# Optimization experiments

Hardware: AMD Instinct MI355X
Metric: run time of the kernel (lower is better)

## Reference

```python
import jax, jax.numpy as jnp
import numpy as np

HIDDEN = 4096
NUM_HEADS = 32
NUM_KV_HEADS = 8
HEAD_DIM = HIDDEN // NUM_HEADS  # 128
Q_SIZE = NUM_HEADS * HEAD_DIM    # 4096
KV_SIZE = NUM_KV_HEADS * HEAD_DIM  # 1024
SCALE = 1.0 / HEAD_DIM  # attention_multiplier=None -> head_dim ** (-1)
ROPE_BASE = 10000.0


def _rope_neox(x, positions):
    # x: [B, S, H, D], positions: [B, S] int
    half = HEAD_DIM // 2
    inv_freq = 1.0 / (ROPE_BASE ** (jnp.arange(0, half, dtype=jnp.float32) / half))
    freqs = positions.astype(jnp.float32)[..., None] * inv_freq  # [B, S, half]
    cos = jnp.cos(freqs)[:, :, None, :]  # [B, S, 1, half]
    sin = jnp.sin(freqs)[:, :, None, :]
    x1, x2 = x[..., :half], x[..., half:]
    return jnp.concatenate([x1 * cos - x2 * sin, x2 * cos + x1 * sin], axis=-1)


def setup_inputs() -> dict:
    key = jax.random.key(0)
    k1, k2, k3 = jax.random.split(key, 3)
    B, S = 2, 2048
    positions = jnp.broadcast_to(jnp.arange(S, dtype=jnp.int32), (B, S))
    hidden_states = jax.random.normal(k1, (B, S, HIDDEN), dtype=jnp.float32) * 0.02
    w_qkv = jax.random.normal(k2, (Q_SIZE + 2 * KV_SIZE, HIDDEN), dtype=jnp.float32) * 0.02
    w_o = jax.random.normal(k3, (HIDDEN, Q_SIZE), dtype=jnp.float32) * 0.02
    return {"positions": positions, "hidden_states": hidden_states, "w_qkv": w_qkv, "w_o": w_o}


def reference(positions, hidden_states, w_qkv, w_o):
    B, S, _ = hidden_states.shape
    # fused QKV projection
    qkv = jnp.einsum('bsh,oh->bso', hidden_states, w_qkv)
    q = qkv[..., :Q_SIZE].reshape(B, S, NUM_HEADS, HEAD_DIM)
    k = qkv[..., Q_SIZE:Q_SIZE + KV_SIZE].reshape(B, S, NUM_KV_HEADS, HEAD_DIM)
    v = qkv[..., Q_SIZE + KV_SIZE:].reshape(B, S, NUM_KV_HEADS, HEAD_DIM)
    # neox-style RoPE on q and k
    q = _rope_neox(q, positions)
    k = _rope_neox(k, positions)
    # GQA: repeat kv heads
    rep = NUM_HEADS // NUM_KV_HEADS
    k = jnp.repeat(k, rep, axis=2)  # [B, S, NUM_HEADS, D]
    v = jnp.repeat(v, rep, axis=2)
    # causal attention
    scores = jnp.einsum('bqhd,bkhd->bhqk', q, k) * SCALE
    causal = jnp.tril(jnp.ones((S, S), dtype=bool))
    scores = jnp.where(causal, scores, jnp.finfo(scores.dtype).min)
    probs = jax.nn.softmax(scores, axis=-1)
    attn = jnp.einsum('bhqk,bkhd->bqhd', probs, v).reshape(B, S, Q_SIZE)
    # output projection
    return jnp.einsum('bsq,hq->bsh', attn, w_o)
```

## Files before the change

### kernel.cpp

```cpp
#include <hip/hip_runtime.h>
#include <hip/hip_bf16.h>
#include <cmath>

typedef __bf16 bf16x8 __attribute__((ext_vector_type(8)));
typedef __bf16 bf16x4 __attribute__((ext_vector_type(4)));
typedef float  f32x4  __attribute__((ext_vector_type(4)));
typedef unsigned int u32;
typedef u32 u32x4 __attribute__((ext_vector_type(4)));

#define AS1 __attribute__((address_space(1)))
#define AS3 __attribute__((address_space(3)))
#define GLDS16(gp, lp) __builtin_amdgcn_global_load_lds((AS1 void*)(gp), (AS3 void*)(lp), 16, 0, 0)

#define B_DIM 2
#define S_LEN 2048
#define HIDDEN 4096
#define NHEADS 32
#define NKV 8
#define HDIM 128
#define QSZ 4096
#define KVSZ 1024
#define QKVSZ 6144
#define GK 4096
#define ATT_SCALE 0.0078125f
#define L2E 1.4426950408889634f

__global__ __launch_bounds__(256) void conv_f32_bf16(const float* __restrict__ in,
                                                     __bf16* __restrict__ out, int n4) {
    int idx = blockIdx.x * 256 + threadIdx.x;
    if (idx < n4) {
        float4 v = ((const float4*)in)[idx];
        bf16x4 o;
        o[0] = (__bf16)v.x; o[1] = (__bf16)v.y; o[2] = (__bf16)v.z; o[3] = (__bf16)v.w;
        ((bf16x4*)out)[idx] = o;
    }
}

__global__ __launch_bounds__(256) void rope_table_kernel(float* __restrict__ ct,
                                                         float* __restrict__ st) {
    int idx = blockIdx.x * 256 + threadIdx.x;
    int p = idx >> 6, i = idx & 63;
    float inv = expf(-(float)i * (9.210340371976184f / 64.0f));
    float freq = (float)p * inv;
    float s, c;
    sincosf(freq, &s, &c);
    ct[idx] = c; st[idx] = s;
}

template<typename OUT>
__global__ __launch_bounds__(512, 2) void gemm256(const __bf16* __restrict__ A,
                                                  const __bf16* __restrict__ B,
                                                  OUT* __restrict__ C,
                                                  int N) {
    __shared__ __bf16 Asm[2 * 16384 + 2 * 16384];
    char* Bbase = (char*)Asm + 65536;

    const int tid = threadIdx.x;
    const int w = tid >> 6, l = tid & 63;
    const int l15 = l & 15, l4 = l >> 4;
    const int wr = w >> 2, wc = w & 3;

    const int nwg = gridDim.x * gridDim.y;
    const int orig = blockIdx.y * gridDim.x + blockIdx.x;
    const int swz = (orig & 7) * (nwg >> 3) + (orig >> 3);
    const int bx = swz % gridDim.x, by = swz / gridDim.x;
    const int m0 = by * 256, n0 = bx * 256;

    const __bf16* Ag = A + (size_t)m0 * GK;
    const __bf16* Bg = B + (size_t)n0 * GK;

#define STAGE_AQ(q, tile) do {                                                  \
        int c_ = (q) * 512 + tid;                                               \
        int r_ = c_ >> 3;                                                       \
        int jg_ = (tid & 7) ^ (r_ & 7);                                         \
        GLDS16(Ag + (size_t)r_ * GK + (tile) * 64 + jg_ * 8,                    \
               (char*)Asm + ((tile) & 1) * 32768 + c_ * 16);                    \
    } while (0)
#define STAGE_BS(s, tile) do {                                                  \
        _Pragma("unroll")                                                       \
        for (int i_ = 0; i_ < 2; ++i_) {                                        \
            int v_ = i_ * 512 + tid;                                            \
            int r_ = (v_ >> 8) * 64 + (s) * 32 + ((v_ >> 3) & 31);              \
            int jg_ = (v_ & 7) ^ (r_ & 7);                                      \
            int c_ = r_ * 8 + (v_ & 7);                                         \
            GLDS16(Bg + (size_t)r_ * GK + (tile) * 64 + jg_ * 8,                \
                   Bbase + ((tile) & 1) * 32768 + c_ * 16);                     \
        }                                                                       \
    } while (0)

#define LOAD_A(DST, MH) do {                                                    \
        _Pragma("unroll")                                                       \
        for (int m2 = 0; m2 < 4; ++m2) {                                        \
            int row = wr * 128 + ((MH) * 4 + m2) * 16 + l15;                    \
            _Pragma("unroll")                                                   \
            for (int kk = 0; kk < 2; ++kk) {                                    \
                int j = (kk * 4 + l4) ^ (row & 7);                              \
                DST[m2][kk] = *(const bf16x8*)(Als + row * 64 + j * 8);         \
            }                                                                   \
        }                                                                       \
    } while (0)
#define LOAD_B(DST, NH) do {                                                    \
        _Pragma("unroll")                                                       \
        for (int n2 = 0; n2 < 2; ++n2) {                                        \
            int row = wc * 64 + ((NH) * 2 + n2) * 16 + l15;                     \
            _Pragma("unroll")                                                   \
            for (int kk = 0; kk < 2; ++kk) {                                    \
                int j = (kk * 4 + l4) ^ (row & 7);                              \
                DST[n2][kk] = *(const bf16x8*)(Bls + row * 64 + j * 8);         \
            }                                                                   \
        }                                                                       \
    } while (0)
#define MFMA_QUAD(AF, BF, MI0, NI0)                                             \
    _Pragma("unroll")                                                           \
    for (int m2 = 0; m2 < 4; ++m2)                                              \
        _Pragma("unroll")                                                       \
        for (int n2 = 0; n2 < 2; ++n2)                                          \
            _Pragma("unroll")                                                   \
            for (int kk = 0; kk < 2; ++kk)                                      \
                acc[(MI0) + m2][(NI0) + n2] =                                   \
                    __builtin_amdgcn_mfma_f32_16x16x32_bf16(                    \
                        AF[m2][kk], BF[n2][kk], acc[(MI0) + m2][(NI0) + n2], 0, 0, 0);
#define PH_SYNC_PRE  do { __builtin_amdgcn_sched_barrier(0);                    \
        __builtin_amdgcn_s_barrier();                                           \
        asm volatile("s_waitcnt lgkmcnt(0)" ::: "memory");                      \
        __builtin_amdgcn_sched_barrier(0); } while (0)
#define PH_SYNC_POST do { __builtin_amdgcn_sched_barrier(0);                    \
        __builtin_amdgcn_s_barrier(); } while (0)

    f32x4 acc[8][4] = {};

    const int T = GK / 64;
    STAGE_AQ(0, 0); STAGE_AQ(1, 0); STAGE_AQ(2, 0); STAGE_AQ(3, 0);
    STAGE_BS(0, 0); STAGE_BS(1, 0);
    STAGE_AQ(0, 1); STAGE_AQ(2, 1); STAGE_BS(0, 1);
    asm volatile("s_waitcnt vmcnt(4)" ::: "memory");
    __builtin_amdgcn_s_barrier();

    for (int t = 0; t < T; ++t) {
        const __bf16* Als = Asm + (t & 1) * 16384;
        const __bf16* Bls = (__bf16*)Bbase + (t & 1) * 16384;
        bf16x8 af0[4][2], af1[4][2], bfr[2][2];
        LOAD_A(af0, 0);
        LOAD_B(bfr, 0);
        if (t + 1 < T) { STAGE_AQ(1, t + 1); STAGE_AQ(3, t + 1); }
        PH_SYNC_PRE;
        __builtin_amdgcn_s_setprio(1);
        MFMA_QUAD(af0, bfr, 0, 0);
        __builtin_amdgcn_s_setprio(0);
        PH_SYNC_POST;
        LOAD_B(bfr, 1);
        if (t + 1 < T) STAGE_BS(1, t + 1);
        PH_SYNC_PRE;
        __builtin_amdgcn_s_setprio(1);
        MFMA_QUAD(af0, bfr, 0, 2);
        __builtin_amdgcn_s_setprio(0);
        PH_SYNC_POST;
        LOAD_A(af1, 1);
        LOAD_B(bfr, 0);
        if (t + 2 < T) { STAGE_AQ(0, t + 2); STAGE_AQ(2, t + 2); }
        PH_SYNC_PRE;
        __builtin_amdgcn_s_setprio(1);
        MFMA_QUAD(af1, bfr, 4, 0);
        __builtin_amdgcn_s_setprio(0);
        PH_SYNC_POST;
        LOAD_B(bfr, 1);
        if (t + 2 < T) STAGE_BS(0, t + 2);
        PH_SYNC_PRE;
        __builtin_amdgcn_s_setprio(1);
        MFMA_QUAD(af1, bfr, 4, 2);
        __builtin_amdgcn_s_setprio(0);
        if (t + 2 < T)      { asm volatile("s_waitcnt vmcnt(4)" ::: "memory"); }
        else if (t + 1 < T) { asm volatile("s_waitcnt vmcnt(0)" ::: "memory"); }
        PH_SYNC_POST;
    }
#undef PH_SYNC_PRE
#undef PH_SYNC_POST
#undef MFMA_QUAD
#undef LOAD_A
#undef LOAD_B
#undef STAGE_AQ
#undef STAGE_BS

#pragma unroll
    for (int mi = 0; mi < 8; ++mi)
#pragma unroll
        for (int ni = 0; ni < 4; ++ni)
#pragma unroll
            for (int r = 0; r < 4; ++r)
                C[(size_t)(m0 + wr * 128 + mi * 16 + l4 * 4 + r) * N
                  + n0 + wc * 64 + ni * 16 + l15] = (OUT)acc[mi][ni][r];
}

__global__ __launch_bounds__(256) void rope_kernel(const __bf16* __restrict__ qkv,
                                                   const int* __restrict__ pos,
                                                   const float* __restrict__ ct,
                                                   const float* __restrict__ st,
                                                   __bf16* __restrict__ Qb,
                                                   __bf16* __restrict__ Kb) {
    const int tid = threadIdx.x;
    const int tok = blockIdx.x;
    const int b = tok >> 11, s = tok & 2047;
    const int p = pos[tok];
    const __bf16* base = qkv + (size_t)tok * QKVSZ;
    const float* cb = ct + (size_t)p * 64;
    const float* sb = st + (size_t)p * 64;
    for (int idx = tid; idx < 2560; idx += 256) {
        int head = idx >> 6, i = idx & 63;
        float c = cb[i], sn = sb[i];
        if (head < 32) {
            float x1 = (float)base[head * HDIM + i];
            float x2 = (float)base[head * HDIM + 64 + i];
            size_t o = ((size_t)(b * 32 + head) * S_LEN + s) * HDIM + i;
            Qb[o]      = (__bf16)((x1 * c - x2 * sn) * ATT_SCALE);
            Qb[o + 64] = (__bf16)((x2 * c + x1 * sn) * ATT_SCALE);
        } else {
            int g = head - 32;
            float x1 = (float)base[QSZ + g * HDIM + i];
            float x2 = (float)base[QSZ + g * HDIM + 64 + i];
            size_t o = ((size_t)(b * 8 + g) * S_LEN + s) * HDIM + i;
            Kb[o]      = (__bf16)(x1 * c - x2 * sn);
            Kb[o + 64] = (__bf16)(x2 * c + x1 * sn);
        }
    }
}

__global__ __launch_bounds__(256) void vtrans_kernel(const __bf16* __restrict__ qkv,
                                                     __bf16* __restrict__ Vt) {
    __shared__ __bf16 T[64][132];
    const int tid = threadIdx.x;
    const int st = blockIdx.x, g = blockIdx.y, b = blockIdx.z;
    const __bf16* src = qkv + ((size_t)(b * S_LEN + st * 64)) * QKVSZ + (QSZ + KVSZ) + g * HDIM;
#pragma unroll
    for (int it = 0; it < 8; ++it) {
        int c = it * 256 + tid;
        int row = c >> 5;
        int c4 = c & 31;
        bf16x4 v = *(const bf16x4*)(src + (size_t)row * QKVSZ + c4 * 4);
        *(bf16x4*)(&T[row][c4 * 4]) = v;
    }
    __syncthreads();
#pragma unroll
    for (int it = 0; it < 8; ++it) {
        int c = it * 256 + tid;
        int d = c >> 4;
        int s4 = (c & 15) * 4;
        bf16x4 o;
        o[0] = T[s4 + 0][d]; o[1] = T[s4 + 1][d]; o[2] = T[s4 + 2][d]; o[3] = T[s4 + 3][d];
        *(bf16x4*)(Vt + ((size_t)(b * 8 + g) * HDIM + d) * S_LEN + st * 64 + s4) = o;
    }
}

__global__ __launch_bounds__(256, 2) void attn_kernel(const __bf16* __restrict__ Q,
                                                      const __bf16* __restrict__ K,
                                                      const __bf16* __restrict__ Vt,
                                                      __bf16* __restrict__ O) {
    const int tid = threadIdx.x;
    const int w = tid >> 6, l = tid & 63;
    const int l15 = l & 15, l4 = l >> 4;
    const int qt = gridDim.x - 1 - blockIdx.x;
    const int h = blockIdx.y, b = blockIdx.z;
    const int g = h >> 2;
    const int qw0 = qt * 128 + w * 32;

    __shared__ __bf16 Ks[2][64 * 128];
    __shared__ __bf16 Vs[2][128 * 64];

    const __bf16* Qp = Q + ((size_t)((b * 32 + h) * S_LEN + qw0)) * HDIM;
    const __bf16* Kp = K + (size_t)(b * 8 + g) * S_LEN * HDIM;
    const __bf16* Vp = Vt + (size_t)(b * 8 + g) * HDIM * S_LEN;

    bf16x8 qf[2][4];
#pragma unroll
    for (int qh = 0; qh < 2; ++qh)
#pragma unroll
        for (int kk = 0; kk < 4; ++kk)
            qf[qh][kk] = *(const bf16x8*)(Qp + (size_t)(qh * 16 + l15) * HDIM + kk * 32 + l4 * 8);

    f32x4 acc[2][8] = {};
    float m[2]    = {-1e30f, -1e30f};
    float lsum[2] = {0.f, 0.f};
    const bool oddl4 = (l4 & 1);

#define STAGE(buf, ktile) do {                                                     \
        const __bf16* kbase = Kp + (size_t)(ktile) * 64 * HDIM;                    \
        _Pragma("unroll")                                                          \
        for (int i_ = 0; i_ < 4; ++i_) {                                           \
            int c_ = i_ * 256 + tid;                \
            int row_ = c_ >> 4, cc_ = (c_ & 15) ^ (row_ & 7);                      \
            GLDS16(kbase + (size_t)row_ * HDIM + cc_ * 8,                          \
                   (char*)Ks[buf] + c_ * 16);                                      \
        }                                                                          \
        const __bf16* vbase = Vp + (size_t)(ktile) * 64;                           \
        _Pragma("unroll")                                                          \
        for (int i_ = 0; i_ < 4; ++i_) {                                           \
            int c_ = i_ * 256 + tid;                \
            int row_ = c_ >> 3, cc_ = (c_ & 7) ^ (row_ & 7);                       \
            GLDS16(vbase + (size_t)row_ * S_LEN + cc_ * 8,                         \
                   (char*)Vs[buf] + c_ * 16);                                      \
        }                                                                          \
    } while (0)

    const int nkt = 2 * qt + 2;
    int cur = 0;
    STAGE(0, 0);
    __syncthreads();

    for (int kt = 0; kt < nkt; ++kt) {
        if (kt + 1 < nkt) STAGE(cur ^ 1, kt + 1);
        if (kt * 64 <= qw0 + 31) {
            f32x4 sfr[2][4];
            __builtin_amdgcn_s_setprio(1);
#pragma unroll
            for (int fn = 0; fn < 4; ++fn) {
                f32x4 sa0 = {}, sa1 = {};
#pragma unroll
                for (int kk = 0; kk < 4; ++kk) {
                    int row = fn * 16 + l15;
                    int cc = (kk * 4 + l4) ^ (l15 & 7);
                    bf16x8 kb = *(const bf16x8*)(Ks[cur] + row * HDIM + cc * 8);
                    sa0 = __builtin_amdgcn_mfma_f32_16x16x32_bf16(kb, qf[0][kk], sa0, 0, 0, 0);
                    sa1 = __builtin_amdgcn_mfma_f32_16x16x32_bf16(kb, qf[1][kk], sa1, 0, 0, 0);
                }
                sfr[0][fn] = sa0; sfr[1][fn] = sa1;
            }
            __builtin_amdgcn_s_setprio(0);
            const bool needmask = (kt * 64 + 63 > qw0);
            bf16x8 pb[2][2];
#pragma unroll
            for (int qh = 0; qh < 2; ++qh) {
                const int qrow = qw0 + qh * 16 + l15;
                float pmax = -1e30f;
#pragma unroll
                for (int fn = 0; fn < 4; ++fn)
#pragma unroll
                    for (int r = 0; r < 4; ++r) {
                        float v = sfr[qh][fn][r];
                        if (needmask) {
                            int kcol = kt * 64 + fn * 16 + l4 * 4 + r;
                            if (kcol > qrow) v = -1e30f;
                        }
                        sfr[qh][fn][r] = v;
                        pmax = fmaxf(pmax, v);
                    }
                pmax = fmaxf(pmax, __shfl_xor(pmax, 16));
                pmax = fmaxf(pmax, __shfl_xor(pmax, 32));
                if (!__all(pmax - m[qh] <= 8.0f)) {
                    float mn = fmaxf(m[qh], pmax);
                    float alpha = exp2f((m[qh] - mn) * L2E);
                    m[qh] = mn;
                    lsum[qh] *= alpha;
#pragma unroll
                    for (int n = 0; n < 8; ++n)
#pragma unroll
                        for (int r = 0; r < 4; ++r) acc[qh][n][r] *= alpha;
                }
                float rs = 0.f;
                u32 pk01[4], pk23[4];
#pragma unroll
                for (int fn = 0; fn < 4; ++fn) {
                    float p0 = exp2f((sfr[qh][fn][0] - m[qh]) * L2E);
                    float p1 = exp2f((sfr[qh][fn][1] - m[qh]) * L2E);
                    float p2 = exp2f((sfr[qh][fn][2] - m[qh]) * L2E);
                    float p3 = exp2f((sfr[qh][fn][3] - m[qh]) * L2E);
                    rs += (p0 + p1) + (p2 + p3);
                    asm("v_cvt_pk_bf16_f32 %0, %1, %2" : "=v"(pk01[fn]) : "v"(p0), "v"(p1));
                    asm("v_cvt_pk_bf16_f32 %0, %1, %2" : "=v"(pk23[fn]) : "v"(p2), "v"(p3));
                }
                rs += __shfl_xor(rs, 16);
                rs += __shfl_xor(rs, 32);
                lsum[qh] += rs;
#pragma unroll
                for (int kk = 0; kk < 2; ++kk) {
                    u32 a01 = pk01[2 * kk],     a23 = pk23[2 * kk];
                    u32 b01 = pk01[2 * kk + 1], b23 = pk23[2 * kk + 1];
                    asm("v_permlane32_swap_b32 %0, %1" : "+v"(a01), "+v"(b01));
                    asm("v_permlane32_swap_b32 %0, %1" : "+v"(a23), "+v"(b23));
                    u32 oa01 = __shfl_xor(a01, 16);
                    u32 oa23 = __shfl_xor(a23, 16);
                    u32 ob01 = __shfl_xor(b01, 16);
                    u32 ob23 = __shfl_xor(b23, 16);
                    u32x4 wv;
                    wv[0] = oddl4 ? ob01 : a01;
                    wv[1] = oddl4 ? ob23 : a23;
                    wv[2] = oddl4 ? b01 : oa01;
                    wv[3] = oddl4 ? b23 : oa23;
                    pb[qh][kk] = __builtin_bit_cast(bf16x8, wv);
                }
            }
            __builtin_amdgcn_s_setprio(1);
#pragma unroll
            for (int kk = 0; kk < 2; ++kk) {
#pragma unroll
                for (int n = 0; n < 8; ++n) {
                    int row = n * 16 + l15;
                    int cc = (kk * 4 + l4) ^ (l15 & 7);
                    bf16x8 vb = *(const bf16x8*)(Vs[cur] + row * 64 + cc * 8);
                    acc[0][n] = __builtin_amdgcn_mfma_f32_16x16x32_bf16(vb, pb[0][kk], acc[0][n], 0, 0, 0);
                    acc[1][n] = __builtin_amdgcn_mfma_f32_16x16x32_bf16(vb, pb[1][kk], acc[1][n], 0, 0, 0);
                }
            }
            __builtin_amdgcn_s_setprio(0);
        }
        __syncthreads();
        cur ^= 1;
    }
#undef STAGE
#pragma unroll
    for (int qh = 0; qh < 2; ++qh) {
        float inv = 1.0f / lsum[qh];
        int qrow = qw0 + qh * 16 + l15;
        __bf16* obase = O + ((size_t)(b * S_LEN) + qrow) * QSZ + h * HDIM + l4 * 4;
#pragma unroll
        for (int n = 0; n < 8; ++n) {
            bf16x4 o4;
#pragma unroll
            for (int r = 0; r < 4; ++r) o4[r] = (__bf16)(acc[qh][n][r] * inv);
            *(bf16x4*)(obase + n * 16) = o4;
        }
    }
}

extern "C" void kernel_launch(void* const* d_in, const int* in_sizes, int n_in,
                              void* d_out, int out_size, void* d_ws, size_t ws_size,
                              hipStream_t stream) {
    const int*   pos    = (const int*)d_in[0];
    const float* hidden = (const float*)d_in[1];
    const float* wqkv   = (const float*)d_in[2];
    const float* wo     = (const float*)d_in[3];
    float* out = (float*)d_out;

    __bf16* hb    = (__bf16*)d_ws;
    __bf16* wqb   = hb  + 16777216;
    __bf16* wob   = wqb + 25165824;
    __bf16* qkv   = wob + 16777216;
    __bf16* Qb    = qkv + 25165824;
    __bf16* Kb    = Qb  + 16777216;
    __bf16* Vtb   = Kb  + 4194304;
    __bf16* attnb = Vtb + 4194304;
    float*  rc    = (float*)(attnb + 16777216);
    float*  rs    = rc + 131072;

    conv_f32_bf16<<<16384, 256, 0, stream>>>(hidden, hb, 4194304);
    conv_f32_bf16<<<24576, 256, 0, stream>>>(wqkv, wqb, 6291456);
    conv_f32_bf16<<<16384, 256, 0, stream>>>(wo, wob, 4194304);
    rope_table_kernel<<<512, 256, 0, stream>>>(rc, rs);
    gemm256<__bf16><<<dim3(QKVSZ / 256, (B_DIM * S_LEN) / 256), 512, 0, stream>>>(hb, wqb, qkv, QKVSZ);
    rope_kernel<<<B_DIM * S_LEN, 256, 0, stream>>>(qkv, pos, rc, rs, Qb, Kb);
    vtrans_kernel<<<dim3(S_LEN / 64, NKV, B_DIM), 256, 0, stream>>>(qkv, Vtb);
    attn_kernel<<<dim3(S_LEN / 128, NHEADS, B_DIM), 256, 0, stream>>>(Qb, Kb, Vtb, attnb);
    gemm256<float><<<dim3(HIDDEN / 256, (B_DIM * S_LEN) / 256), 512, 0, stream>>>(attnb, wob, out, HIDDEN);
}
```

Before: 625.6 us.

## Enlarge attention query tile to 256 rows with 8 waves and use permlane reductions

The attention kernel now runs 512 threads per block and covers 256 query rows, so each staged K/V tile in shared memory is reused by twice as many waves and the cooperative load work per thread is halved. Row max and sum reductions and the P-fragment repacking switch from ds_swizzle/shfl_xor cross-lane ops to v_permlane16/32_swap instructions, which removes the select logic. The cost is fewer blocks in the grid and coarser causal load imbalance, since the waves covering early rows of a tile sit idle through the later key tiles. Occupancy may also change under the 512-thread launch bound.

Result: no change. 628.6 us (+0.5%).

```diff
diff --git a/kernel.cpp b/kernel.cpp
--- a/kernel.cpp
+++ b/kernel.cpp
@@ -250,7 +250,7 @@
     }
 }
 
-__global__ __launch_bounds__(256, 2) void attn_kernel(const __bf16* __restrict__ Q,
+__global__ __launch_bounds__(512, 2) void attn_kernel(const __bf16* __restrict__ Q,
                                                       const __bf16* __restrict__ K,
                                                       const __bf16* __restrict__ Vt,
                                                       __bf16* __restrict__ O) {
@@ -260,7 +260,7 @@
     const int qt = gridDim.x - 1 - blockIdx.x;
     const int h = blockIdx.y, b = blockIdx.z;
     const int g = h >> 2;
-    const int qw0 = qt * 128 + w * 32;
+    const int qw0 = qt * 256 + w * 32;
 
     __shared__ __bf16 Ks[2][64 * 128];
     __shared__ __bf16 Vs[2][128 * 64];
@@ -279,28 +279,41 @@
     f32x4 acc[2][8] = {};
     float m[2]    = {-1e30f, -1e30f};
     float lsum[2] = {0.f, 0.f};
-    const bool oddl4 = (l4 & 1);
+
+#define RED16(x, OPINS) do {                                                      \
+        u32 ra_ = __builtin_bit_cast(u32, x), rb_;                                \
+        asm("v_mov_b32 %0, %1" : "=v"(rb_) : "v"(ra_));                           \
+        asm("v_permlane16_swap_b32 %0, %1" : "+v"(ra_), "+v"(rb_));               \
+        x = OPINS(__builtin_bit_cast(float, ra_), __builtin_bit_cast(float, rb_));\
+    } while (0)
+#define RED32(x, OPINS) do {                                                      \
+        u32 ra_ = __builtin_bit_cast(u32, x), rb_;                                \
+        asm("v_mov_b32 %0, %1" : "=v"(rb_) : "v"(ra_));                           \
+        asm("v_permlane32_swap_b32 %0, %1" : "+v"(ra_), "+v"(rb_));               \
+        x = OPINS(__builtin_bit_cast(float, ra_), __builtin_bit_cast(float, rb_));\
+    } while (0)
+#define FADD_(a_, b_) ((a_) + (b_))
 
 #define STAGE(buf, ktile) do {                                                     \
         const __bf16* kbase = Kp + (size_t)(ktile) * 64 * HDIM;                    \
         _Pragma("unroll")                                                          \
-        for (int i_ = 0; i_ < 4; ++i_) {                                           \
-            int c_ = i_ * 256 + tid;                \
+        for (int i_ = 0; i_ < 2; ++i_) {                                           \
+            int c_ = i_ * 512 + tid;                \
             int row_ = c_ >> 4, cc_ = (c_ & 15) ^ (row_ & 7);                      \
             GLDS16(kbase + (size_t)row_ * HDIM + cc_ * 8,                          \
                    (char*)Ks[buf] + c_ * 16);                                      \
         }                                                                          \
         const __bf16* vbase = Vp + (size_t)(ktile) * 64;                           \
         _Pragma("unroll")                                                          \
-        for (int i_ = 0; i_ < 4; ++i_) {                                           \
-            int c_ = i_ * 256 + tid;                \
+        for (int i_ = 0; i_ < 2; ++i_) {                                           \
+            int c_ = i_ * 512 + tid;                \
             int row_ = c_ >> 3, cc_ = (c_ & 7) ^ (row_ & 7);                       \
             GLDS16(vbase + (size_t)row_ * S_LEN + cc_ * 8,                         \
                    (char*)Vs[buf] + c_ * 16);                                      \
         }                                                                          \
     } while (0)
 
-    const int nkt = 2 * qt + 2;
+    const int nkt = 4 * qt + 4;
     int cur = 0;
     STAGE(0, 0);
     __syncthreads();
@@ -342,8 +355,8 @@
                         sfr[qh][fn][r] = v;
                         pmax = fmaxf(pmax, v);
                     }
-                pmax = fmaxf(pmax, __shfl_xor(pmax, 16));
-                pmax = fmaxf(pmax, __shfl_xor(pmax, 32));
+                RED16(pmax, fmaxf);
+                RED32(pmax, fmaxf);
                 if (!__all(pmax - m[qh] <= 8.0f)) {
                     float mn = fmaxf(m[qh], pmax);
                     float alpha = exp2f((m[qh] - mn) * L2E);
@@ -366,24 +379,19 @@
                     asm("v_cvt_pk_bf16_f32 %0, %1, %2" : "=v"(pk01[fn]) : "v"(p0), "v"(p1));
                     asm("v_cvt_pk_bf16_f32 %0, %1, %2" : "=v"(pk23[fn]) : "v"(p2), "v"(p3));
                 }
-                rs += __shfl_xor(rs, 16);
-                rs += __shfl_xor(rs, 32);
+                RED16(rs, FADD_);
+                RED32(rs, FADD_);
                 lsum[qh] += rs;
 #pragma unroll
                 for (int kk = 0; kk < 2; ++kk) {
-                    u32 a01 = pk01[2 * kk],     a23 = pk23[2 * kk];
-                    u32 b01 = pk01[2 * kk + 1], b23 = pk23[2 * kk + 1];
-                    asm("v_permlane32_swap_b32 %0, %1" : "+v"(a01), "+v"(b01));
-                    asm("v_permlane32_swap_b32 %0, %1" : "+v"(a23), "+v"(b23));
-                    u32 oa01 = __shfl_xor(a01, 16);
-                    u32 oa23 = __shfl_xor(a23, 16);
-                    u32 ob01 = __shfl_xor(b01, 16);
-                    u32 ob23 = __shfl_xor(b23, 16);
+                    u32 w0 = pk01[2 * kk], w2 = pk01[2 * kk + 1];
+                    asm("v_permlane32_swap_b32 %0, %1" : "+v"(w0), "+v"(w2));
+                    asm("v_permlane16_swap_b32 %0, %1" : "+v"(w0), "+v"(w2));
+                    u32 w1 = pk23[2 * kk], w3 = pk23[2 * kk + 1];
+                    asm("v_permlane32_swap_b32 %0, %1" : "+v"(w1), "+v"(w3));
+                    asm("v_permlane16_swap_b32 %0, %1" : "+v"(w1), "+v"(w3));
                     u32x4 wv;
-                    wv[0] = oddl4 ? ob01 : a01;
-                    wv[1] = oddl4 ? ob23 : a23;
-                    wv[2] = oddl4 ? b01 : oa01;
-                    wv[3] = oddl4 ? b23 : oa23;
+                    wv[0] = w0; wv[1] = w1; wv[2] = w2; wv[3] = w3;
                     pb[qh][kk] = __builtin_bit_cast(bf16x8, wv);
                 }
             }
@@ -405,6 +413,9 @@
         cur ^= 1;
     }
 #undef STAGE
+#undef RED16
+#undef RED32
+#undef FADD_
 #pragma unroll
     for (int qh = 0; qh < 2; ++qh) {
         float inv = 1.0f / lsum[qh];
@@ -447,6 +458,6 @@
     gemm256<__bf16><<<dim3(QKVSZ / 256, (B_DIM * S_LEN) / 256), 512, 0, stream>>>(hb, wqb, qkv, QKVSZ);
     rope_kernel<<<B_DIM * S_LEN, 256, 0, stream>>>(qkv, pos, rc, rs, Qb, Kb);
     vtrans_kernel<<<dim3(S_LEN / 64, NKV, B_DIM), 256, 0, stream>>>(qkv, Vtb);
-    attn_kernel<<<dim3(S_LEN / 128, NHEADS, B_DIM), 256, 0, stream>>>(Qb, Kb, Vtb, attnb);
+    attn_kernel<<<dim3(S_LEN / 256, NHEADS, B_DIM), 512, 0, stream>>>(Qb, Kb, Vtb, attnb);
     gemm256<float><<<dim3(HIDDEN / 256, (B_DIM * S_LEN) / 256), 512, 0, stream>>>(attnb, wob, out, HIDDEN);
 }
```
